# Kernel optimization log

Hardware: AMD Instinct MI355X
Metric: run time of the kernel (lower is better)

## Reference

```python
import jax, jax.numpy as jnp
import numpy as np

DIM = 1024
N_HEADS = 16
HEAD_DIM = DIM // N_HEADS  # 64
THETA = 10000.0
B, S = 4, 1024


def _rope_full_dim(x):
    """RoPE applied over the FULL last dim (head_dim == model dim), matching the
    original module which builds RotaryEmbeddings(head_dim=args.dim) and applies
    it to [B, S, dim] before splitting into heads. Positions start at 0."""
    Bx, Sx, D = x.shape
    freq = 1.0 / (THETA ** (jnp.arange(0, D, 2, dtype=jnp.float32) / D))  # [D/2]
    ang = jnp.arange(Sx, dtype=jnp.float32)[:, None] * freq[None, :]      # [S, D/2]
    cos, sin = jnp.cos(ang), jnp.sin(ang)
    xp = x.astype(jnp.float32).reshape(Bx, Sx, D // 2, 2)
    x0, x1 = xp[..., 0], xp[..., 1]
    rot = jnp.stack([x0 * cos - x1 * sin, x0 * sin + x1 * cos], axis=-1)
    return rot.reshape(Bx, Sx, D).astype(x.dtype)


def setup_inputs() -> dict:
    key = jax.random.key(0)
    ks = jax.random.split(key, 5)
    scale = 1.0 / np.sqrt(DIM)
    x = jax.random.normal(ks[0], (B, S, DIM), dtype=jnp.float32)
    Wq = jax.random.normal(ks[1], (DIM, DIM), dtype=jnp.float32) * scale
    Wk = jax.random.normal(ks[2], (DIM, DIM), dtype=jnp.float32) * scale
    Wv = jax.random.normal(ks[3], (DIM, DIM), dtype=jnp.float32) * scale
    Wo = jax.random.normal(ks[4], (DIM, DIM), dtype=jnp.float32) * scale
    bo = jnp.zeros((DIM,), dtype=jnp.float32)
    return {"x": x, "Wq": Wq, "Wk": Wk, "Wv": Wv, "Wo": Wo, "bo": bo, "start_pos": 0}


def reference(x, Wq, Wk, Wv, Wo, bo, start_pos):
    # start_pos == 0: the zero-initialized KV cache write+read is an identity
    # (keys == xk, values == xv over [:, :S]); n_rep == 1 so repeat_kv is a no-op.
    # NOTE: the original applies NO causal mask.
    Bx, Sx, _ = x.shape
    xq = _rope_full_dim(x @ Wq.T)  # [B, S, DIM] (weights stored torch-style [out,in])
    xk = _rope_full_dim(x @ Wk.T)
    xv = x @ Wv.T
    q = xq.reshape(Bx, Sx, N_HEADS, HEAD_DIM).transpose(0, 2, 1, 3)  # [B,H,S,D]
    k = xk.reshape(Bx, Sx, N_HEADS, HEAD_DIM).transpose(0, 2, 1, 3)
    v = xv.reshape(Bx, Sx, N_HEADS, HEAD_DIM).transpose(0, 2, 1, 3)
    scores = jnp.einsum("bhqd,bhkd->bhqk", q, k) / np.float32(np.sqrt(HEAD_DIM))
    attn = jax.nn.softmax(scores.astype(jnp.float32), axis=-1).astype(q.dtype)
    out = jnp.einsum("bhqk,bhkd->bhqd", attn, v)          # [B,H,S,D]
    out = out.transpose(0, 2, 1, 3).reshape(Bx, Sx, DIM)  # [B,S,DIM]
    return out @ Wo.T + bo
```

## Files before the change

### kernel.cpp

```cpp
#include <hip/hip_runtime.h>
#include <cstdint>
#include <cstddef>

typedef _Float16 f16;
typedef __attribute__((ext_vector_type(8))) _Float16 h8v;
typedef __attribute__((ext_vector_type(4))) _Float16 h4v;
typedef __attribute__((ext_vector_type(4))) float f4v;

#define DIM 1024
#define SEQ 1024
#define NH 16
#define HD 64

__device__ __forceinline__ void gld16(const void* g, void* l) {
  __builtin_amdgcn_global_load_lds(
      (const __attribute__((address_space(1))) void*)g,
      (__attribute__((address_space(3))) void*)l, 16, 0, 0);
}

__device__ __forceinline__ f4v mfma16(h8v a, h8v b, f4v c) {
  return __builtin_amdgcn_mfma_f32_16x16x32_f16(a, b, c, 0, 0, 0);
}
__device__ __forceinline__ f4v mfma16k16(h4v a, h4v b, f4v c) {
  return __builtin_amdgcn_mfma_f32_16x16x16f16(a, b, c, 0, 0, 0);
}

__device__ __forceinline__ void cvt_store4(f16* dst, float4 v) {
  *(h4v*)dst = (h4v){(f16)v.x, (f16)v.y, (f16)v.z, (f16)v.w};
}

__global__ __launch_bounds__(256) void convert_kernel(
    const float* __restrict__ x,  const float* __restrict__ Wq,
    const float* __restrict__ Wk, const float* __restrict__ Wv,
    const float* __restrict__ Wo,
    f16* __restrict__ xh, f16* __restrict__ wqkv, f16* __restrict__ woh)
{
  int i = blockIdx.x * 256 + threadIdx.x;
  cvt_store4(xh + 4 * (size_t)i, ((const float4*)x)[i]);
  if (i < DIM * DIM / 4) {
    cvt_store4(wqkv + 4 * (size_t)i,               ((const float4*)Wq)[i]);
    cvt_store4(wqkv + DIM * DIM + 4 * (size_t)i,   ((const float4*)Wk)[i]);
    cvt_store4(wqkv + 2 * DIM * DIM + 4 * (size_t)i, ((const float4*)Wv)[i]);
    cvt_store4(woh + 4 * (size_t)i,                ((const float4*)Wo)[i]);
  }
}

__global__ __launch_bounds__(256) void qkv_gemm(
    const f16* __restrict__ A, const f16* __restrict__ W,
    f16* __restrict__ Qh, f16* __restrict__ Kh, f16* __restrict__ Vt)
{
  __shared__ f16 lA[128 * 32];
  __shared__ f16 lB[128 * 32];
  const int m0 = blockIdx.x * 128;
  const int n0 = blockIdx.y * 128;
  const int tid = threadIdx.x;
  const int w = tid >> 6, lane = tid & 63, quad = lane >> 4, l16 = lane & 15;
  const int wm = (w >> 1) * 64, wn = (w & 1) * 64;

  const int c0 = tid, c1 = 256 + tid;
  const int r0 = c0 >> 2, kc0 = (c0 & 3) ^ ((r0 >> 1) & 3);
  const int r1 = c1 >> 2, kc1 = (c1 & 3) ^ ((r1 >> 1) & 3);
  const f16* gA0 = A + (size_t)(m0 + r0) * DIM + kc0 * 8;
  const f16* gA1 = A + (size_t)(m0 + r1) * DIM + kc1 * 8;
  const f16* gB0 = W + (size_t)(n0 + r0) * DIM + kc0 * 8;
  const f16* gB1 = W + (size_t)(n0 + r1) * DIM + kc1 * 8;
  f16* lA0 = &lA[(c0 & ~63) * 8];
  f16* lA1 = &lA[(c1 & ~63) * 8];
  f16* lB0 = &lB[(c0 & ~63) * 8];
  f16* lB1 = &lB[(c1 & ~63) * 8];

  int pA[4], pB[4];
#pragma unroll
  for (int t = 0; t < 4; ++t) {
    int r = wm + t * 16 + l16;
    pA[t] = r * 4 + (quad ^ ((r >> 1) & 3));
    int rn = wn + t * 16 + l16;
    pB[t] = rn * 4 + (quad ^ ((rn >> 1) & 3));
  }

  f4v acc[4][4] = {};
  for (int kt = 0; kt < DIM / 32; ++kt) {
    const int ko = kt * 32;
    gld16(gA0 + ko, lA0);
    gld16(gA1 + ko, lA1);
    gld16(gB0 + ko, lB0);
    gld16(gB1 + ko, lB1);
    __syncthreads();
    h8v af[4], bf[4];
#pragma unroll
    for (int t = 0; t < 4; ++t) af[t] = *(const h8v*)&lA[pA[t] * 8];
#pragma unroll
    for (int t = 0; t < 4; ++t) bf[t] = *(const h8v*)&lB[pB[t] * 8];
#pragma unroll
    for (int i = 0; i < 4; ++i)
#pragma unroll
      for (int j = 0; j < 4; ++j)
        acc[i][j] = mfma16(af[i], bf[j], acc[i][j]);
    __syncthreads();
  }

  if (n0 < 2 * DIM) {
    f16* dst = (n0 < DIM) ? Qh : Kh;
#pragma unroll
    for (int i = 0; i < 4; ++i) {
      const int mb = m0 + wm + i * 16 + quad * 4;
#pragma unroll
      for (int j = 0; j < 4; ++j) {
        const int n = n0 + wn + j * 16 + l16;
        const int d = n & (DIM - 1);
        const float fr = exp2f(-0.025952563f * (float)(d >> 1));
        const float sgn = (d & 1) ? 1.0f : -1.0f;
        const int hh = d >> 6, dd = d & 63;
#pragma unroll
        for (int r = 0; r < 4; ++r) {
          const int m = mb + r;
          const int s = m & (SEQ - 1), b = m >> 10;
          const float v = acc[i][j][r];
          const float pt = __shfl_xor(v, 1, 64);
          float sn, cs;
          __sincosf((float)s * fr, &sn, &cs);
          dst[((size_t)(b * NH + hh) * SEQ + s) * HD + dd] =
              (f16)(v * cs + sgn * pt * sn);
        }
      }
    }
  } else {
#pragma unroll
    for (int i = 0; i < 4; ++i) {
      const int mb = m0 + wm + i * 16 + quad * 4;
      const int s = mb & (SEQ - 1), b = mb >> 10;
#pragma unroll
      for (int j = 0; j < 4; ++j) {
        const int d = (n0 - 2 * DIM) + wn + j * 16 + l16;
        const int hh = d >> 6, dd = d & 63;
        h4v vv = {(f16)acc[i][j][0], (f16)acc[i][j][1],
                  (f16)acc[i][j][2], (f16)acc[i][j][3]};
        *(h4v*)&Vt[((size_t)(b * NH + hh) * HD + dd) * SEQ + s] = vv;
      }
    }
  }
}

__global__ __launch_bounds__(256) void attn_kernel(
    const f16* __restrict__ Q, const f16* __restrict__ K,
    const f16* __restrict__ V, f16* __restrict__ O)
{
  __shared__ f16 lK[64 * 64];
  __shared__ f16 lV[64 * 64];
  const int tid = threadIdx.x;
  const int w = tid >> 6, lane = tid & 63, quad = lane >> 4, l16 = lane & 15;
  const int qt = blockIdx.x, bh = blockIdx.y;
  const f16* Qb = Q + (size_t)bh * SEQ * HD;
  const f16* Kb = K + (size_t)bh * SEQ * HD;
  const f16* Vb = V + (size_t)bh * HD * SEQ;
  const int q0 = qt * 64;
  const int qrow = q0 + w * 16 + l16;

  h8v bq0 = *(const h8v*)&Qb[(size_t)qrow * HD + quad * 8];
  h8v bq1 = *(const h8v*)&Qb[(size_t)qrow * HD + quad * 8 + 32];
  bq0 = bq0 * (f16)0.125f;
  bq1 = bq1 * (f16)0.125f;

  const int c0 = tid, c1 = 256 + tid;
  const int r0 = c0 >> 3, kc0 = (c0 & 7) ^ (r0 & 7);
  const int r1 = c1 >> 3, kc1 = (c1 & 7) ^ (r1 & 7);
  const f16* gK0 = Kb + (size_t)r0 * HD + kc0 * 8;
  const f16* gK1 = Kb + (size_t)r1 * HD + kc1 * 8;
  const f16* gV0 = Vb + (size_t)r0 * SEQ + kc0 * 8;
  const f16* gV1 = Vb + (size_t)r1 * SEQ + kc1 * 8;
  f16* lK0 = &lK[(c0 & ~63) * 8];
  f16* lK1 = &lK[(c1 & ~63) * 8];
  f16* lV0 = &lV[(c0 & ~63) * 8];
  f16* lV1 = &lV[(c1 & ~63) * 8];

  int pbt[4][2];
#pragma unroll
  for (int j = 0; j < 4; ++j) {
    int r = j * 16 + l16;
#pragma unroll
    for (int kk = 0; kk < 2; ++kk)
      pbt[j][kk] = r * 8 + ((quad + 4 * kk) ^ (r & 7));
  }
  const f16* vbase[4];
#pragma unroll
  for (int j = 0; j < 4; ++j) {
    int slot = (j * 2 + (quad >> 1)) ^ (l16 & 7);
    vbase[j] = &lV[l16 * 64 + slot * 8 + (quad & 1) * 4];
  }

  float mr = -1e30f, lr = 0.f;
  f4v accO[4] = {};

  for (int t = 0; t < SEQ / 64; ++t) {
    const int key0 = t * 64;
    __syncthreads();
    gld16(gK0 + (size_t)key0 * HD, lK0);
    gld16(gK1 + (size_t)key0 * HD, lK1);
    gld16(gV0 + key0, lV0);
    gld16(gV1 + key0, lV1);
    __syncthreads();

    f4v sc[4];
#pragma unroll
    for (int j = 0; j < 4; ++j) {
      f4v z = {};
      z = mfma16(*(const h8v*)&lK[pbt[j][0] * 8], bq0, z);
      z = mfma16(*(const h8v*)&lK[pbt[j][1] * 8], bq1, z);
      sc[j] = z;
    }

    float tm = sc[0][0];
#pragma unroll
    for (int j = 0; j < 4; ++j)
#pragma unroll
      for (int r = 0; r < 4; ++r) tm = fmaxf(tm, sc[j][r]);
    tm = fmaxf(tm, __shfl_xor(tm, 16, 64));
    tm = fmaxf(tm, __shfl_xor(tm, 32, 64));
    const float mnew = fmaxf(mr, tm);
    const float alpha = __expf(mr - mnew);
    mr = mnew;

    float p[4][4];
    float rs = 0.f;
#pragma unroll
    for (int j = 0; j < 4; ++j)
#pragma unroll
      for (int r = 0; r < 4; ++r) {
        p[j][r] = __expf(sc[j][r] - mnew);
        rs += p[j][r];
      }
    rs += __shfl_xor(rs, 16, 64);
    rs += __shfl_xor(rs, 32, 64);
    lr = lr * alpha + rs;

    f4v av;
#pragma unroll
    for (int r = 0; r < 4; ++r) av[r] = __shfl(alpha, quad * 4 + r, 64);
#pragma unroll
    for (int dt = 0; dt < 4; ++dt) accO[dt] *= av;

    h4v pf[4];
#pragma unroll
    for (int j = 0; j < 4; ++j)
      pf[j] = (h4v){(f16)p[j][0], (f16)p[j][1], (f16)p[j][2], (f16)p[j][3]};

#pragma unroll
    for (int dt = 0; dt < 4; ++dt)
#pragma unroll
      for (int j = 0; j < 4; ++j)
        accO[dt] = mfma16k16(pf[j], *(const h4v*)(vbase[j] + dt * 1024),
                             accO[dt]);
  }

  f4v invl;
#pragma unroll
  for (int r = 0; r < 4; ++r) invl[r] = 1.0f / __shfl(lr, quad * 4 + r, 64);

  const int b = bh >> 4, hh = bh & 15;
#pragma unroll
  for (int dt = 0; dt < 4; ++dt) {
    const int d = dt * 16 + l16;
#pragma unroll
    for (int r = 0; r < 4; ++r) {
      const int s = q0 + w * 16 + quad * 4 + r;
      O[(size_t)(b * SEQ + s) * DIM + hh * HD + d] = (f16)(accO[dt][r] * invl[r]);
    }
  }
}

__global__ __launch_bounds__(256) void out_gemm(
    const f16* __restrict__ A, const f16* __restrict__ W,
    const float* __restrict__ bias, float* __restrict__ out)
{
  __shared__ f16 lA[64 * 32];
  __shared__ f16 lB[128 * 32];
  const int m0 = blockIdx.x * 64;
  const int n0 = blockIdx.y * 128;
  const int tid = threadIdx.x;
  const int w = tid >> 6, lane = tid & 63, quad = lane >> 4, l16 = lane & 15;
  const int wm = (w >> 1) * 32, wn = (w & 1) * 64;

  const int c0 = tid, c1 = 256 + tid;
  const int rA = c0 >> 2, kcA = (c0 & 3) ^ ((rA >> 1) & 3);
  const int rB1 = c1 >> 2, kcB1 = (c1 & 3) ^ ((rB1 >> 1) & 3);
  const f16* gA  = A + (size_t)(m0 + rA) * DIM + kcA * 8;
  const f16* gB0 = W + (size_t)(n0 + rA) * DIM + kcA * 8;
  const f16* gB1 = W + (size_t)(n0 + rB1) * DIM + kcB1 * 8;
  f16* lAp  = &lA[(c0 & ~63) * 8];
  f16* lB0p = &lB[(c0 & ~63) * 8];
  f16* lB1p = &lB[(c1 & ~63) * 8];

  int pA_[2], pB_[4];
#pragma unroll
  for (int t = 0; t < 2; ++t) {
    int r = wm + t * 16 + l16;
    pA_[t] = r * 4 + (quad ^ ((r >> 1) & 3));
  }
#pragma unroll
  for (int t = 0; t < 4; ++t) {
    int rn = wn + t * 16 + l16;
    pB_[t] = rn * 4 + (quad ^ ((rn >> 1) & 3));
  }

  f4v acc[2][4] = {};
  for (int kt = 0; kt < DIM / 32; ++kt) {
    const int ko = kt * 32;
    gld16(gA + ko, lAp);
    gld16(gB0 + ko, lB0p);
    gld16(gB1 + ko, lB1p);
    __syncthreads();
    h8v af[2], bf[4];
#pragma unroll
    for (int t = 0; t < 2; ++t) af[t] = *(const h8v*)&lA[pA_[t] * 8];
#pragma unroll
    for (int t = 0; t < 4; ++t) bf[t] = *(const h8v*)&lB[pB_[t] * 8];
#pragma unroll
    for (int i = 0; i < 2; ++i)
#pragma unroll
      for (int j = 0; j < 4; ++j)
        acc[i][j] = mfma16(af[i], bf[j], acc[i][j]);
    __syncthreads();
  }

#pragma unroll
  for (int i = 0; i < 2; ++i) {
#pragma unroll
    for (int j = 0; j < 4; ++j) {
      const int n = n0 + wn + j * 16 + l16;
      const float bv = bias[n];
#pragma unroll
      for (int r = 0; r < 4; ++r) {
        const int m = m0 + wm + i * 16 + quad * 4 + r;
        out[(size_t)m * DIM + n] = acc[i][j][r] + bv;
      }
    }
  }
}

extern "C" void kernel_launch(void* const* d_in, const int* in_sizes, int n_in,
                              void* d_out, int out_size, void* d_ws, size_t ws_size,
                              hipStream_t stream)
{
  (void)in_sizes; (void)n_in; (void)out_size; (void)ws_size;
  const float* x  = (const float*)d_in[0];
  const float* Wq = (const float*)d_in[1];
  const float* Wk = (const float*)d_in[2];
  const float* Wv = (const float*)d_in[3];
  const float* Wo = (const float*)d_in[4];
  const float* bo = (const float*)d_in[5];
  float* out = (float*)d_out;

  char* ws = (char*)d_ws;
  const size_t MB = (size_t)1 << 20;
  f16* xh   = (f16*)(ws);
  f16* wqkv = (f16*)(ws + 8  * MB);
  f16* woh  = (f16*)(ws + 14 * MB);
  f16* Qh   = (f16*)(ws + 16 * MB);
  f16* Kh   = (f16*)(ws + 24 * MB);
  f16* Vt   = (f16*)(ws + 32 * MB);
  f16* Oh   = (f16*)(ws);

  convert_kernel<<<dim3(4096), 256, 0, stream>>>(x, Wq, Wk, Wv, Wo, xh, wqkv, woh);
  qkv_gemm<<<dim3(32, 24), 256, 0, stream>>>(xh, wqkv, Qh, Kh, Vt);
  attn_kernel<<<dim3(16, 64), 256, 0, stream>>>(Qh, Kh, Vt, Oh);
  out_gemm<<<dim3(64, 8), 256, 0, stream>>>(Oh, woh, bo, out);
}
```

Measured before the change: 181.0 us.

## Double-buffer K/V tiles in attention and fold softmax scale into Q

After: 181.5 us. Within noise of the previous version (+0.3%).

```diff
diff --git a/kernel.cpp b/kernel.cpp
--- a/kernel.cpp
+++ b/kernel.cpp
@@ -101,6 +101,7 @@
 
   if (n0 < 2 * DIM) {
     f16* dst = (n0 < DIM) ? Qh : Kh;
+    const float osc = (n0 < DIM) ? 0.18033688f : 1.0f;
 #pragma unroll
     for (int i = 0; i < 4; ++i) {
       const int mb = m0 + wm + i * 16 + quad * 4;
@@ -120,7 +121,7 @@
           float sn, cs;
           __sincosf((float)s * fr, &sn, &cs);
           dst[((size_t)(b * NH + hh) * SEQ + s) * HD + dd] =
-              (f16)(v * cs + sgn * pt * sn);
+              (f16)((v * cs + sgn * pt * sn) * osc);
         }
       }
     }
@@ -145,67 +146,73 @@
     const f16* __restrict__ Q, const f16* __restrict__ K,
     const f16* __restrict__ V, f16* __restrict__ O)
 {
-  __shared__ f16 lK[64 * 64];
-  __shared__ f16 lV[64 * 64];
+  __shared__ f16 lbuf[2][8192];
   const int tid = threadIdx.x;
   const int w = tid >> 6, lane = tid & 63, quad = lane >> 4, l16 = lane & 15;
   const int qt = blockIdx.x, bh = blockIdx.y;
   const f16* Qb = Q + (size_t)bh * SEQ * HD;
-  const f16* Kb = K + (size_t)bh * SEQ * HD;
-  const f16* Vb = V + (size_t)bh * HD * SEQ;
+  const f16* Kg = K + (size_t)bh * SEQ * HD;
+  const f16* Vg = V + (size_t)bh * HD * SEQ;
   const int q0 = qt * 64;
   const int qrow = q0 + w * 16 + l16;
 
-  h8v bq0 = *(const h8v*)&Qb[(size_t)qrow * HD + quad * 8];
-  h8v bq1 = *(const h8v*)&Qb[(size_t)qrow * HD + quad * 8 + 32];
-  bq0 = bq0 * (f16)0.125f;
-  bq1 = bq1 * (f16)0.125f;
+  const h8v bq0 = *(const h8v*)&Qb[(size_t)qrow * HD + quad * 8];
+  const h8v bq1 = *(const h8v*)&Qb[(size_t)qrow * HD + quad * 8 + 32];
 
   const int c0 = tid, c1 = 256 + tid;
   const int r0 = c0 >> 3, kc0 = (c0 & 7) ^ (r0 & 7);
   const int r1 = c1 >> 3, kc1 = (c1 & 7) ^ (r1 & 7);
-  const f16* gK0 = Kb + (size_t)r0 * HD + kc0 * 8;
-  const f16* gK1 = Kb + (size_t)r1 * HD + kc1 * 8;
-  const f16* gV0 = Vb + (size_t)r0 * SEQ + kc0 * 8;
-  const f16* gV1 = Vb + (size_t)r1 * SEQ + kc1 * 8;
-  f16* lK0 = &lK[(c0 & ~63) * 8];
-  f16* lK1 = &lK[(c1 & ~63) * 8];
-  f16* lV0 = &lV[(c0 & ~63) * 8];
-  f16* lV1 = &lV[(c1 & ~63) * 8];
-
-  int pbt[4][2];
+  const f16* gK0 = Kg + (size_t)r0 * HD + kc0 * 8;
+  const f16* gK1 = Kg + (size_t)r1 * HD + kc1 * 8;
+  const f16* gV0 = Vg + (size_t)r0 * SEQ + kc0 * 8;
+  const f16* gV1 = Vg + (size_t)r1 * SEQ + kc1 * 8;
+  const int dk0 = (c0 & ~63) * 8, dk1 = (c1 & ~63) * 8;
+
+  int koff[4][2];
 #pragma unroll
   for (int j = 0; j < 4; ++j) {
     int r = j * 16 + l16;
 #pragma unroll
     for (int kk = 0; kk < 2; ++kk)
-      pbt[j][kk] = r * 8 + ((quad + 4 * kk) ^ (r & 7));
-  }
-  const f16* vbase[4];
+      koff[j][kk] = (r * 8 + ((quad + 4 * kk) ^ (r & 7))) * 8;
+  }
+  int voff[4];
 #pragma unroll
   for (int j = 0; j < 4; ++j) {
     int slot = (j * 2 + (quad >> 1)) ^ (l16 & 7);
-    vbase[j] = &lV[l16 * 64 + slot * 8 + (quad & 1) * 4];
+    voff[j] = 4096 + l16 * 64 + slot * 8 + (quad & 1) * 4;
   }
 
   float mr = -1e30f, lr = 0.f;
   f4v accO[4] = {};
 
+  {
+    f16* base = lbuf[0];
+    gld16(gK0, base + dk0);
+    gld16(gK1, base + dk1);
+    gld16(gV0, base + 4096 + dk0);
+    gld16(gV1, base + 4096 + dk1);
+  }
+
   for (int t = 0; t < SEQ / 64; ++t) {
-    const int key0 = t * 64;
-    __syncthreads();
-    gld16(gK0 + (size_t)key0 * HD, lK0);
-    gld16(gK1 + (size_t)key0 * HD, lK1);
-    gld16(gV0 + key0, lV0);
-    gld16(gV1 + key0, lV1);
-    __syncthreads();
+    const int b = t & 1;
+    __syncthreads();
+    if (t + 1 < SEQ / 64) {
+      const size_t key0 = (size_t)(t + 1) * 64;
+      f16* base = lbuf[b ^ 1];
+      gld16(gK0 + key0 * HD, base + dk0);
+      gld16(gK1 + key0 * HD, base + dk1);
+      gld16(gV0 + key0, base + 4096 + dk0);
+      gld16(gV1 + key0, base + 4096 + dk1);
+    }
+    const f16* L = lbuf[b];
 
     f4v sc[4];
 #pragma unroll
     for (int j = 0; j < 4; ++j) {
       f4v z = {};
-      z = mfma16(*(const h8v*)&lK[pbt[j][0] * 8], bq0, z);
-      z = mfma16(*(const h8v*)&lK[pbt[j][1] * 8], bq1, z);
+      z = mfma16(*(const h8v*)&L[koff[j][0]], bq0, z);
+      z = mfma16(*(const h8v*)&L[koff[j][1]], bq1, z);
       sc[j] = z;
     }
 
@@ -217,7 +224,16 @@
     tm = fmaxf(tm, __shfl_xor(tm, 16, 64));
     tm = fmaxf(tm, __shfl_xor(tm, 32, 64));
     const float mnew = fmaxf(mr, tm);
-    const float alpha = __expf(mr - mnew);
+
+    if (__any(mnew > mr)) {
+      const float alpha = exp2f(mr - mnew);
+      lr *= alpha;
+      f4v av;
+#pragma unroll
+      for (int r = 0; r < 4; ++r) av[r] = __shfl(alpha, quad * 4 + r, 64);
+#pragma unroll
+      for (int dt = 0; dt < 4; ++dt) accO[dt] *= av;
+    }
     mr = mnew;
 
     float p[4][4];
@@ -226,18 +242,12 @@
     for (int j = 0; j < 4; ++j)
 #pragma unroll
       for (int r = 0; r < 4; ++r) {
-        p[j][r] = __expf(sc[j][r] - mnew);
+        p[j][r] = exp2f(sc[j][r] - mnew);
         rs += p[j][r];
       }
     rs += __shfl_xor(rs, 16, 64);
     rs += __shfl_xor(rs, 32, 64);
-    lr = lr * alpha + rs;
-
-    f4v av;
-#pragma unroll
-    for (int r = 0; r < 4; ++r) av[r] = __shfl(alpha, quad * 4 + r, 64);
-#pragma unroll
-    for (int dt = 0; dt < 4; ++dt) accO[dt] *= av;
+    lr += rs;
 
     h4v pf[4];
 #pragma unroll
@@ -248,7 +258,7 @@
     for (int dt = 0; dt < 4; ++dt)
 #pragma unroll
       for (int j = 0; j < 4; ++j)
-        accO[dt] = mfma16k16(pf[j], *(const h4v*)(vbase[j] + dt * 1024),
+        accO[dt] = mfma16k16(pf[j], *(const h4v*)&L[voff[j] + dt * 1024],
                              accO[dt]);
   }
 
```
